# Kernel optimization log

Measured on AMD Instinct MI355X. Metric: run time of the kernel, lower is better.

## Reference

```python
import jax, jax.numpy as jnp
import numpy as np
from jax import lax

NAG = 3          # hardcoded in the torch module (query slices, catted_torches)
B = 4096         # batch_size per agent
H = 128          # hidden_dim
HEADS = 8
AD = H // HEADS  # attend_dim
STATE, ACT, SCAN = 48, 2, 256
OUTF, HID = 10, 256
NFEAT = 32 * (SCAN - 6)  # conv output features (two VALID convs: k5 then k3)
EPS = 1e-5

def leaky(x):
    return jnp.where(x >= 0, x, 0.01 * x)

def setup_inputs() -> dict:
    key = jax.random.key(0)
    ks = iter(jax.random.split(key, 40))
    def rn(shape, scale=0.05):
        return jax.random.normal(next(ks), shape, dtype=jnp.float32) * scale
    return {
        'obs':  jax.random.normal(next(ks), (NAG * B, STATE), jnp.float32),
        'acts': jax.random.normal(next(ks), (NAG * B, ACT), jnp.float32),
        'scan': jax.random.normal(next(ks), (NAG * B, SCAN), jnp.float32),
        'conv_w1': rn((32, 1, 5)),  'conv_b1': jnp.zeros((32,), jnp.float32),
        'conv_w2': rn((32, 32, 3)), 'conv_b2': jnp.zeros((32,), jnp.float32),
        'fc_w1': rn((256, NFEAT), 0.01), 'fc_b1': jnp.zeros((256,), jnp.float32),
        'fc_w2': rn((OUTF, 256)),        'fc_b2': jnp.zeros((OUTF,), jnp.float32),
        'enc_w': rn((H, STATE + ACT + OUTF)), 'enc_b': jnp.zeros((H,), jnp.float32),
        'Wk': rn((HEADS, AD, H)),
        'Wv': rn((HEADS, AD, H)), 'bv': jnp.zeros((HEADS, AD), jnp.float32),
        'Wq': rn((NAG, HEADS, AD, H)),
        'q1_w1': rn((HID, 2 * H)), 'q1_b1': jnp.zeros((HID,), jnp.float32),
        'q1_w2': rn((HID, HID)),   'q1_b2': jnp.zeros((HID,), jnp.float32),
        'q1_w3': rn((1, HID)),     'q1_b3': jnp.zeros((1,), jnp.float32),
        'q2_w1': rn((HID, 2 * H)), 'q2_b1': jnp.zeros((HID,), jnp.float32),
        'q2_w2': rn((HID, HID)),   'q2_b2': jnp.zeros((HID,), jnp.float32),
        'q2_w3': rn((1, HID)),     'q2_b3': jnp.zeros((1,), jnp.float32),
    }

def reference(obs, acts, scan, conv_w1, conv_b1, conv_w2, conv_b2,
              fc_w1, fc_b1, fc_w2, fc_b2, enc_w, enc_b, Wk, Wv, bv, Wq,
              q1_w1, q1_b1, q1_w2, q1_b2, q1_w3, q1_b3,
              q2_w1, q2_b1, q2_w2, q2_b2, q2_w3, q2_b3):
    dn = ('NCH', 'OIH', 'NCH')
    x = scan[:, None, :]                                            # [N,1,L]
    x = lax.conv_general_dilated(x, conv_w1, (1,), 'VALID', dimension_numbers=dn)
    x = jax.nn.relu(x + conv_b1[None, :, None])
    x = lax.conv_general_dilated(x, conv_w2, (1,), 'VALID', dimension_numbers=dn)
    x = jax.nn.relu(x + conv_b2[None, :, None])
    x = x.reshape(x.shape[0], -1)                                   # [N, NFEAT]
    x = jax.nn.relu(x @ fc_w1.T + fc_b1)
    feats = x @ fc_w2.T + fc_b2                                     # [N, OUTF]

    inps = jnp.concatenate([obs, acts, feats], axis=1)
    mu, var = inps.mean(0), inps.var(0)                             # BatchNorm1d (train, no affine)
    normed = (inps - mu) / jnp.sqrt(var + EPS)
    sa = leaky(normed @ enc_w.T + enc_b).reshape(NAG, B, H)         # [ag,B,H]

    keys = jnp.einsum('gbh,ndh->ngbd', sa, Wk)                      # [hd,ag,B,ad]
    vals = leaky(jnp.einsum('gbh,ndh->ngbd', sa, Wv) + bv[:, None, None, :])
    q = jnp.einsum('gbh,gndh->gnbd', sa, Wq)                        # [ag,hd,B,ad]

    logits = jnp.einsum('gnbd,nobd->gnbo', q, keys) / np.sqrt(AD)   # [ag,hd,B,ag]
    self_mask = jnp.eye(NAG, dtype=bool)[:, None, None, :]          # exclude own agent
    logits = jnp.where(self_mask, -jnp.inf, logits)
    w = jax.nn.softmax(logits, axis=-1)
    other = jnp.einsum('gnbo,nobd->gnbd', w, vals)                  # [ag,hd,B,ad]
    other = other.transpose(0, 2, 1, 3).reshape(NAG, B, H)          # heads concatenated

    emb = jnp.concatenate([sa, other], axis=2).reshape(NAG * B, 2 * H)

    def mlp(x, w1, b1, w2, b2, w3, b3):
        x = jax.nn.relu(x @ w1.T + b1)
        x = jax.nn.relu(x @ w2.T + b2)
        return x @ w3.T + b3

    q1 = mlp(emb, q1_w1, q1_b1, q1_w2, q1_b2, q1_w3, q1_b3)
    q2 = mlp(emb, q2_w1, q2_b1, q2_w2, q2_b2, q2_w3, q2_b3)
    return (q1, q2)
```

## Files before the change

kernel.cpp:

```cpp
#include <hip/hip_runtime.h>
#include <hip/hip_bf16.h>
#include <cstdint>
#include <cstddef>

typedef unsigned short u16;
typedef __attribute__((ext_vector_type(8))) __bf16 bf16x8;
typedef __attribute__((ext_vector_type(4))) float f32x4;

__device__ __forceinline__ u16 f2b(float f) {
  __hip_bfloat16 h = __float2bfloat16(f);
  return *reinterpret_cast<u16*>(&h);
}
__device__ __forceinline__ uint32_t pk2(float a, float b) {
  __hip_bfloat162 h = __float22bfloat162_rn(make_float2(a, b));
  return *reinterpret_cast<uint32_t*>(&h);
}
__device__ __forceinline__ float b2f(u16 u) {
  union { float f; uint32_t i; } x; x.i = ((uint32_t)u) << 16; return x.f;
}
__device__ __forceinline__ f32x4 mfma16(bf16x8 a, bf16x8 b, f32x4 c) {
  return __builtin_amdgcn_mfma_f32_16x16x32_bf16(a, b, c, 0, 0, 0);
}
__device__ __forceinline__ void async16(const void* g, void* l) {
  __builtin_amdgcn_global_load_lds((const __attribute__((address_space(1))) uint32_t*)g,
                                   (__attribute__((address_space(3))) uint32_t*)l, 16, 0, 0);
}

__global__ __launch_bounds__(256) void w1_perm(const float* __restrict__ w,
                                               u16* __restrict__ o) {
  __shared__ float L[8000];
  int j = blockIdx.x, tid = threadIdx.x;
  for (int i = tid; i < 8000; i += 256) L[i] = w[(size_t)j * 8000 + i];
  __syncthreads();
  for (int i = tid; i < 8000; i += 256) {
    int tt = i >> 5, cc = i & 31;
    int c2 = ((cc >> 2) & 1) * 16 + (cc >> 3) * 4 + (cc & 3);
    o[(size_t)j * 8000 + i] = f2b(L[c2 * 250 + tt]);
  }
}

struct CvtArgs {
  const float* src[15];
  void* dst[15];
  int cum[16];
  int kind[15];
};
__global__ __launch_bounds__(256) void f2b_multi(CvtArgs a, float* stats) {
  int i = blockIdx.x * 256 + threadIdx.x;
  if (blockIdx.x == 0 && threadIdx.x < 128) stats[threadIdx.x] = 0.f;
  int seg = 0;
  #pragma unroll
  for (int s = 1; s < 15; ++s) if (i >= a.cum[s]) seg = s;
  if (i < a.cum[15]) {
    int off = i - a.cum[seg];
    int kind = a.kind[seg];
    const float* src = a.src[seg];
    if (kind == 0) {
      ((u16*)a.dst[seg])[off] = f2b(src[off]);
    } else if (kind == 1) {
      int c2 = off / 96, rem = off - c2 * 96, kk = rem >> 5, c1 = rem & 31;
      ((u16*)a.dst[seg])[off] = f2b(src[(c2 * 32 + c1) * 3 + kk]);
    } else if (kind == 2) {
      int c1 = off >> 5, k = off & 31;
      ((u16*)a.dst[seg])[off] = f2b(k < 5 ? src[c1 * 5 + k] : 0.f);
    } else {
      ((float*)a.dst[seg])[off] = src[off];
    }
  }
}

__global__ __launch_bounds__(256) void conv_fused(
    const float* __restrict__ scan, const u16* __restrict__ w1g,
    const float* __restrict__ cb1, const u16* __restrict__ w2g,
    const float* __restrict__ cb2, u16* __restrict__ x) {
  __shared__ __align__(16) u16 A1[256 * 8];
  __shared__ __align__(16) u16 zbuf[4 * 8];
  __shared__ __align__(16) u16 h1T[258 * 40];
  int tid = threadIdx.x, lane = tid & 63, wv = tid >> 6;
  int l15 = lane & 15, quad = lane >> 4;
  const float* srow = scan + (size_t)blockIdx.x * 256;
  float sv[5];
  #pragma unroll
  for (int k = 0; k < 5; ++k) {
    int p = tid + k;
    sv[k] = (p < 256) ? srow[p] : 0.f;
  }
  union { bf16x8 v; uint32_t d[4]; } pk_;
  pk_.d[0] = pk2(sv[0], sv[1]);
  pk_.d[1] = pk2(sv[2], sv[3]);
  pk_.d[2] = pk2(sv[4], 0.f);
  pk_.d[3] = 0;
  *(bf16x8*)&A1[tid * 8] = pk_.v;
  if (lane < 8) zbuf[wv * 8 + lane] = 0;
  if (tid < 80) h1T[256 * 40 + tid] = 0;
  bf16x8 w1f[2];
  w1f[0] = *(const bf16x8*)&w1g[l15 * 32 + quad * 8];
  w1f[1] = *(const bf16x8*)&w1g[(16 + l15) * 32 + quad * 8];
  bf16x8 w2f[2][3];
  #pragma unroll
  for (int i = 0; i < 2; ++i)
    #pragma unroll
    for (int kk = 0; kk < 3; ++kk)
      w2f[i][kk] = *(const bf16x8*)&w2g[(i * 16 + l15) * 96 + kk * 32 + quad * 8];
  float cb1v[2][4], cb2v[2][4];
  #pragma unroll
  for (int i = 0; i < 2; ++i)
    #pragma unroll
    for (int r = 0; r < 4; ++r) {
      cb1v[i][r] = cb1[i * 16 + quad * 4 + r];
      cb2v[i][r] = cb2[i * 16 + quad * 4 + r];
    }
  asm volatile("s_waitcnt lgkmcnt(0)" ::: "memory");
  f32x4 zero = {0.f, 0.f, 0.f, 0.f};
  {
    f32x4 acc1[4][2];
    #pragma unroll
    for (int nt = 0; nt < 4; ++nt) { acc1[nt][0] = zero; acc1[nt][1] = zero; }
    #pragma unroll
    for (int nt = 0; nt < 4; ++nt) {
      int p = (wv * 4 + nt) * 16 + l15;
      const u16* bp = (quad == 0) ? &A1[p * 8] : &zbuf[wv * 8];
      bf16x8 bfr = *(const bf16x8*)bp;
      acc1[nt][0] = mfma16(w1f[0], bfr, acc1[nt][0]);
      acc1[nt][1] = mfma16(w1f[1], bfr, acc1[nt][1]);
    }
    #pragma unroll
    for (int nt = 0; nt < 4; ++nt) {
      int p = (wv * 4 + nt) * 16 + l15;
      #pragma unroll
      for (int mt = 0; mt < 2; ++mt) {
        float v0 = fmaxf(acc1[nt][mt][0] + cb1v[mt][0], 0.f);
        float v1 = fmaxf(acc1[nt][mt][1] + cb1v[mt][1], 0.f);
        float v2 = fmaxf(acc1[nt][mt][2] + cb1v[mt][2], 0.f);
        float v3 = fmaxf(acc1[nt][mt][3] + cb1v[mt][3], 0.f);
        uint2 u; u.x = pk2(v0, v1); u.y = pk2(v2, v3);
        *(uint2*)&h1T[p * 40 + mt * 16 + quad * 4] = u;
      }
    }
  }
  __syncthreads();
  f32x4 acc2[4][2];
  #pragma unroll
  for (int jj = 0; jj < 4; ++jj) { acc2[jj][0] = zero; acc2[jj][1] = zero; }
  #pragma unroll
  for (int kk = 0; kk < 3; ++kk) {
    #pragma unroll
    for (int jj = 0; jj < 4; ++jj) {
      int t = (wv * 4 + jj) * 16 + l15 + kk;
      bf16x8 h = *(const bf16x8*)&h1T[t * 40 + quad * 8];
      acc2[jj][0] = mfma16(w2f[0][kk], h, acc2[jj][0]);
      acc2[jj][1] = mfma16(w2f[1][kk], h, acc2[jj][1]);
    }
  }
  u16* xr = x + (size_t)blockIdx.x * 8000;
  #pragma unroll
  for (int jj = 0; jj < 4; ++jj) {
    int t = (wv * 4 + jj) * 16 + l15;
    if (t < 250) {
      union { bf16x8 v; uint32_t d[4]; } o_;
      #pragma unroll
      for (int i = 0; i < 2; ++i) {
        float v0 = fmaxf(acc2[jj][i][0] + cb2v[i][0], 0.f);
        float v1 = fmaxf(acc2[jj][i][1] + cb2v[i][1], 0.f);
        float v2 = fmaxf(acc2[jj][i][2] + cb2v[i][2], 0.f);
        float v3 = fmaxf(acc2[jj][i][3] + cb2v[i][3], 0.f);
        o_.d[i * 2]     = pk2(v0, v1);
        o_.d[i * 2 + 1] = pk2(v2, v3);
      }
      *(bf16x8*)&xr[t * 32 + quad * 8] = o_.v;
    }
  }
}

template <int MODE, int MROWS>
__global__ __launch_bounds__(256) void gemm_bt(
    const u16* __restrict__ A, int lda, const u16* __restrict__ W, int ldw,
    const float* __restrict__ bias, float* __restrict__ outF,
    u16* __restrict__ outB, int ldo, int nst, int a_sel, size_t out_zoff,
    const float* __restrict__ w3cat, float* __restrict__ pd) {
  constexpr int AI = (MROWS * 8) / 256;
  __shared__ __align__(16) u16 As[2][MROWS * 64];
  __shared__ __align__(16) u16 Bs[2][128 * 64];
  int tid = threadIdx.x;
  int m0 = blockIdx.y * MROWS;
  int sel = (MODE == 4) ? blockIdx.x : 0;
  int n0 = (MODE == 4) ? 0 : blockIdx.x * 128;
  if (MODE == 4) {
    size_t woff = (sel < 2) ? (size_t)sel * 128 : (size_t)(256 + (m0 >> 12) * 128);
    W += woff * 128;
    outB += (size_t)sel * 12288 * 128;
  }
  if (a_sel) A += (size_t)(blockIdx.x >> 1) * a_sel;
  int kbase = blockIdx.z * nst * 64;
  if (MODE == 0) outF += (size_t)blockIdx.z * out_zoff;
  const u16* Ap = A + (size_t)m0 * lda + kbase;
  const u16* Wp = W + (size_t)n0 * ldw + kbase;
  int lane = tid & 63, wv = tid >> 6;
  int l15 = lane & 15, quad = lane >> 4;
  int wm = (wv >> 1) * (MROWS / 2), wn = (wv & 1) * 64;
  constexpr int MI = MROWS / 32;
  f32x4 zero = {0.f, 0.f, 0.f, 0.f};
  f32x4 acc[MI][4];
  #pragma unroll
  for (int i = 0; i < MI; ++i)
    #pragma unroll
    for (int j = 0; j < 4; ++j) acc[i][j] = zero;

  int sraA[AI], sofA[AI], sdsA[AI];
  #pragma unroll
  for (int it = 0; it < AI; ++it) {
    int c = it * 256 + tid;
    int row = c >> 3, slot = c & 7;
    sraA[it] = row;
    sofA[it] = ((slot ^ (row & 7)) * 8);
    sdsA[it] = c * 8;
  }
  int sraW[4], sofW[4], sdsW[4];
  #pragma unroll
  for (int it = 0; it < 4; ++it) {
    int c = it * 256 + tid;
    int row = c >> 3, slot = c & 7;
    sraW[it] = row;
    sofW[it] = ((slot ^ (row & 7)) * 8);
    sdsW[it] = c * 8;
  }
  int rslot[2];
  rslot[0] = ((quad ^ (l15 & 7)) * 8);
  rslot[1] = (((4 + quad) ^ (l15 & 7)) * 8);

  #pragma unroll 1
  for (int st = 0; st < nst; ++st) {
    if (st == 0) {
      #pragma unroll
      for (int it = 0; it < AI; ++it)
        async16(Ap + (size_t)sraA[it] * lda + sofA[it], &As[0][sdsA[it]]);
      #pragma unroll
      for (int it = 0; it < 4; ++it)
        async16(Wp + (size_t)sraW[it] * ldw + sofW[it], &Bs[0][sdsW[it]]);
    }
    __syncthreads();
    if (st + 1 < nst) {
      const u16* An = Ap + (st + 1) * 64;
      const u16* Wn = Wp + (st + 1) * 64;
      u16* Ad = &As[(st + 1) & 1][0];
      u16* Bd = &Bs[(st + 1) & 1][0];
      #pragma unroll
      for (int it = 0; it < AI; ++it)
        async16(An + (size_t)sraA[it] * lda + sofA[it], Ad + sdsA[it]);
      #pragma unroll
      for (int it = 0; it < 4; ++it)
        async16(Wn + (size_t)sraW[it] * ldw + sofW[it], Bd + sdsW[it]);
    }
    const u16* Ab = &As[st & 1][0];
    const u16* Bb = &Bs[st & 1][0];
    #pragma unroll
    for (int s = 0; s < 2; ++s) {
      bf16x8 af[MI], bfr[4];
      #pragma unroll
      for (int i = 0; i < MI; ++i)
        af[i] = *(const bf16x8*)&Ab[(wm + i * 16 + l15) * 64 + rslot[s]];
      #pragma unroll
      for (int j = 0; j < 4; ++j)
        bfr[j] = *(const bf16x8*)&Bb[(wn + j * 16 + l15) * 64 + rslot[s]];
      #pragma unroll
      for (int i = 0; i < MI; ++i)
        #pragma unroll
        for (int j = 0; j < 4; ++j) acc[i][j] = mfma16(af[i], bfr[j], acc[i][j]);
    }
  }
  if (MODE == 5) {
    float w3v[4], bv4[4];
    #pragma unroll
    for (int j = 0; j < 4; ++j) {
      int n = n0 + wn + j * 16 + l15;
      w3v[j] = w3cat[n];
      bv4[j] = bias[n];
    }
    int sblk = (n0 >> 7) * 2 + (wv & 1);
    #pragma unroll
    for (int i = 0; i < MI; ++i) {
      int mb = m0 + wm + i * 16 + quad * 4;
      #pragma unroll
      for (int r = 0; r < 4; ++r) {
        float s = 0.f;
        #pragma unroll
        for (int j = 0; j < 4; ++j) {
          float v = fmaxf(acc[i][j][r] + bv4[j], 0.f);
          s += v * w3v[j];
        }
        s += __shfl_down(s, 8);
        s += __shfl_down(s, 4);
        s += __shfl_down(s, 2);
        s += __shfl_down(s, 1);
        if (l15 == 0) pd[(size_t)sblk * 12288 + mb + r] = s;
      }
    }
    return;
  }
  #pragma unroll
  for (int i = 0; i < MI; ++i) {
    int mb = m0 + wm + i * 16 + quad * 4;
    #pragma unroll
    for (int j = 0; j < 4; ++j) {
      int n = n0 + wn + j * 16 + l15;
      float bv_ = (MODE == 1 || MODE == 4) ? bias[n] : 0.f;
      #pragma unroll
      for (int r = 0; r < 4; ++r) {
        float v = acc[i][j][r];
        if (MODE == 0) {
          outF[(size_t)(mb + r) * ldo + n] = v;
        } else if (MODE == 1) {
          v = fmaxf(v + bv_, 0.f);
          outB[(size_t)(mb + r) * ldo + n] = f2b(v);
        } else {
          if (sel == 1) { v += bv_; v = v >= 0.f ? v : 0.01f * v; }
          outB[(size_t)(mb + r) * ldo + n] = f2b(v);
        }
      }
    }
  }
}

__global__ __launch_bounds__(256) void fc2_stats(
    const float* __restrict__ hparts, const float* __restrict__ b1,
    const float* __restrict__ w2, const float* __restrict__ b2,
    const float* __restrict__ obs, const float* __restrict__ acts,
    float* __restrict__ inps, float* __restrict__ stats) {
  __shared__ float hL[32 * 260];
  __shared__ float w2L[10 * 260];
  __shared__ float b1L[256];
  __shared__ float ipL[32 * 61];
  int tid = threadIdx.x, r0 = blockIdx.x * 32;
  b1L[tid] = b1[tid];
  for (int i = tid; i < 2560; i += 256) w2L[(i >> 8) * 260 + (i & 255)] = w2[i];
  for (int i = tid; i < 32 * 48; i += 256) {
    int r = i / 48, f = i - r * 48;
    ipL[r * 61 + f] = obs[(size_t)(r0 + r) * 48 + f];
  }
  if (tid < 64) {
    int r = tid >> 1, f = tid & 1;
    ipL[r * 61 + 48 + f] = acts[(size_t)(r0 + r) * 2 + f];
  }
  __syncthreads();
  const size_t HS = (size_t)12288 * 256;
  for (int i = tid; i < 32 * 256; i += 256) {
    int r = i >> 8, c = i & 255;
    size_t g = (size_t)(r0 + r) * 256 + c;
    float v = b1L[c] + hparts[g] + hparts[g + HS] + hparts[g + 2 * HS] +
              hparts[g + 3 * HS] + hparts[g + 4 * HS];
    hL[r * 260 + c] = fmaxf(v, 0.f);
  }
  __syncthreads();
  {
    int r = tid >> 3, ob = tid & 7;
    for (int o = ob; o < 10; o += 8) {
      float a = 0.f;
      #pragma unroll 8
      for (int c = 0; c < 256; ++c) a += hL[r * 260 + c] * w2L[o * 260 + c];
      ipL[r * 61 + 50 + o] = a + b2[o];
    }
  }
  __syncthreads();
  for (int i = tid; i < 32 * 60; i += 256) {
    int r = i / 60, f = i - r * 60;
    inps[(size_t)(r0 + r) * 64 + f] = ipL[r * 61 + f];
  }
  if (tid < 60) {
    float s = 0.f, s2 = 0.f;
    for (int r = 0; r < 32; ++r) {
      float v = ipL[r * 61 + tid];
      s += v; s2 += v * v;
    }
    atomicAdd(&stats[tid], s);
    atomicAdd(&stats[64 + tid], s2);
  }
}

__global__ __launch_bounds__(256) void enc_kernel(
    const float* __restrict__ inps, const float* __restrict__ stats,
    const float* __restrict__ enc_w, const float* __restrict__ enc_b,
    u16* __restrict__ sab) {
  __shared__ float ewL[128 * 61];
  __shared__ float nrm[32 * 61];
  __shared__ float ebL[128];
  __shared__ float muL[60], ivL[60];
  int tid = threadIdx.x, r0 = blockIdx.x * 32;
  if (tid < 128) ebL[tid] = enc_b[tid];
  if (tid < 60) {
    float s = stats[tid], s2 = stats[64 + tid];
    float mu = s * (1.f / 12288.f);
    float var = s2 * (1.f / 12288.f) - mu * mu;
    muL[tid] = mu;
    ivL[tid] = rsqrtf(var + 1e-5f);
  }
  for (int i = tid; i < 128 * 60; i += 256) {
    int h = i / 60, f = i - h * 60;
    ewL[h * 61 + f] = enc_w[i];
  }
  __syncthreads();
  for (int i = tid; i < 32 * 60; i += 256) {
    int r = i / 60, f = i - r * 60;
    nrm[r * 61 + f] = (inps[(size_t)(r0 + r) * 64 + f] - muL[f]) * ivL[f];
  }
  __syncthreads();
  for (int i = tid; i < 32 * 128; i += 256) {
    int r = i >> 7, h = i & 127;
    float a = ebL[h];
    #pragma unroll 4
    for (int f = 0; f < 60; ++f) a += nrm[r * 61 + f] * ewL[h * 61 + f];
    a = a >= 0.f ? a : 0.01f * a;
    sab[(size_t)(r0 + r) * 128 + h] = f2b(a);
  }
}

__global__ __launch_bounds__(128) void attn_combine(
    const u16* __restrict__ qb, const u16* __restrict__ keysb,
    const u16* __restrict__ valsb, const u16* __restrict__ sab,
    u16* __restrict__ emb) {
  __shared__ float qL[3][128], kL[3][128], vL[3][128];
  __shared__ float lg[3][8][3], wgt[3][8][3];
  int b = blockIdx.x, t = threadIdx.x;
  #pragma unroll
  for (int o = 0; o < 3; ++o) {
    size_t base = (size_t)(o * 4096 + b) * 128 + t;
    qL[o][t] = b2f(qb[base]);
    kL[o][t] = b2f(keysb[base]);
    vL[o][t] = b2f(valsb[base]);
  }
  __syncthreads();
  if (t < 72) {
    int g = t / 24, n = (t / 3) % 8, o = t % 3;
    float a = 0.f;
    #pragma unroll
    for (int d = 0; d < 16; ++d) a += qL[g][n * 16 + d] * kL[o][n * 16 + d];
    lg[g][n][o] = (o == g) ? -1e30f : a * 0.25f;
  }
  __syncthreads();
  if (t < 24) {
    int g = t / 8, n = t % 8;
    float m = fmaxf(fmaxf(lg[g][n][0], lg[g][n][1]), lg[g][n][2]);
    float e0 = expf(lg[g][n][0] - m), e1 = expf(lg[g][n][1] - m),
          e2 = expf(lg[g][n][2] - m);
    float inv = 1.f / (e0 + e1 + e2);
    wgt[g][n][0] = e0 * inv; wgt[g][n][1] = e1 * inv; wgt[g][n][2] = e2 * inv;
  }
  __syncthreads();
  int n = t >> 4, d = t & 15;
  #pragma unroll
  for (int g = 0; g < 3; ++g) {
    float o_ = wgt[g][n][0] * vL[0][n * 16 + d] +
               wgt[g][n][1] * vL[1][n * 16 + d] +
               wgt[g][n][2] * vL[2][n * 16 + d];
    size_t rbase = (size_t)(g * 4096 + b) * 256;
    emb[rbase + 128 + t] = f2b(o_);
    emb[rbase + t] = sab[(size_t)(g * 4096 + b) * 128 + t];
  }
}

__global__ __launch_bounds__(256) void final_sum(
    const float* __restrict__ pd, const float* __restrict__ b3a,
    const float* __restrict__ b3b, float* __restrict__ out) {
  int row = blockIdx.x * 256 + threadIdx.x;
  const size_t R = 12288;
  float s1 = pd[row] + pd[R + row] + pd[2 * R + row] + pd[3 * R + row];
  float s2 = pd[4 * R + row] + pd[5 * R + row] + pd[6 * R + row] + pd[7 * R + row];
  out[row] = s1 + b3a[0];
  out[R + row] = s2 + b3b[0];
}

extern "C" void kernel_launch(void* const* d_in, const int* in_sizes, int n_in,
                              void* d_out, int out_size, void* d_ws,
                              size_t ws_size, hipStream_t stream) {
  const float* obs  = (const float*)d_in[0];
  const float* acts = (const float*)d_in[1];
  const float* scan = (const float*)d_in[2];
  const float* cw1  = (const float*)d_in[3];
  const float* cb1  = (const float*)d_in[4];
  const float* cw2  = (const float*)d_in[5];
  const float* cb2  = (const float*)d_in[6];
  const float* fw1  = (const float*)d_in[7];
  const float* fb1  = (const float*)d_in[8];
  const float* fw2  = (const float*)d_in[9];
  const float* fb2  = (const float*)d_in[10];
  const float* encw = (const float*)d_in[11];
  const float* encb = (const float*)d_in[12];
  const float* Wk   = (const float*)d_in[13];
  const float* Wv   = (const float*)d_in[14];
  const float* bv   = (const float*)d_in[15];
  const float* Wq   = (const float*)d_in[16];
  const float* q1w1 = (const float*)d_in[17];
  const float* q1b1 = (const float*)d_in[18];
  const float* q1w2 = (const float*)d_in[19];
  const float* q1b2 = (const float*)d_in[20];
  const float* q1w3 = (const float*)d_in[21];
  const float* q1b3 = (const float*)d_in[22];
  const float* q2w1 = (const float*)d_in[23];
  const float* q2b1 = (const float*)d_in[24];
  const float* q2w2 = (const float*)d_in[25];
  const float* q2b2 = (const float*)d_in[26];
  const float* q2w3 = (const float*)d_in[27];
  const float* q2b3 = (const float*)d_in[28];
  float* out = (float*)d_out;
  char* ws = (char*)d_ws;
  if (ws_size < 264400000u) return;

  u16*   x     = (u16*)(ws + 0);
  u16*   w1b   = (u16*)(ws + 196608000);
  float* hpart = (float*)(ws + 200704000);
  float* stats = (float*)(ws + 263618560);
  u16*   wkvqb = (u16*)(ws + 263619584);
  u16*   m1ab  = (u16*)(ws + 263783424);
  u16*   m2ab  = (u16*)(ws + 264045568);
  u16*   w2g   = (u16*)(ws + 264307712);
  u16*   w1g   = (u16*)(ws + 264313856);
  float* bc1   = (float*)(ws + 264315904);
  float* bc2   = (float*)(ws + 264317952);
  float* w3cat = (float*)(ws + 264320000);
  float* inps  = (float*)(ws + 0);
  u16*   sab   = (u16*)(ws + 3145728);
  u16*   kvqb  = (u16*)(ws + 6291456);
  u16*   embb  = (u16*)(ws + 15728640);
  u16*   t1ab  = (u16*)(ws + 22020096);
  float* pd    = (float*)(ws + 34603008);
  u16*   keysb = kvqb;
  u16*   valsb = kvqb + (size_t)12288 * 128;
  u16*   qb    = kvqb + (size_t)2 * 12288 * 128;

  w1_perm<<<256, 256, 0, stream>>>(fw1, w1b);
  CvtArgs ca;
  const float* srcs[15] = {Wk, Wv, Wq, q1w1, q2w1, q1w2, q2w2, cw2, cw1,
                           q1b1, q2b1, q1b2, q2b2, q1w3, q2w3};
  void* dsts[15] = {wkvqb, wkvqb + 16384, wkvqb + 32768, m1ab, m1ab + 65536,
                    m2ab, m2ab + 65536, w2g, w1g, bc1, bc1 + 256, bc2,
                    bc2 + 256, w3cat, w3cat + 256};
  const int sz[15] = {16384, 16384, 49152, 65536, 65536, 65536, 65536,
                      3072, 1024, 256, 256, 256, 256, 256, 256};
  const int kinds[15] = {0, 0, 0, 0, 0, 0, 0, 1, 2, 3, 3, 3, 3, 3, 3};
  int cum = 0;
  ca.cum[0] = 0;
  for (int i = 0; i < 15; ++i) {
    ca.src[i] = srcs[i]; ca.dst[i] = dsts[i]; ca.kind[i] = kinds[i];
    cum += sz[i]; ca.cum[i + 1] = cum;
  }
  f2b_multi<<<(cum + 255) / 256, 256, 0, stream>>>(ca, stats);

  conv_fused<<<12288, 256, 0, stream>>>(scan, w1g, cb1, w2g, cb2, x);
  gemm_bt<0, 128><<<dim3(2, 96, 5), 256, 0, stream>>>(
      x, 8000, w1b, 8000, nullptr, hpart, nullptr, 256, 25, 0,
      (size_t)12288 * 256, nullptr, nullptr);
  fc2_stats<<<384, 256, 0, stream>>>(hpart, fb1, fw2, fb2, obs, acts, inps, stats);
  enc_kernel<<<384, 256, 0, stream>>>(inps, stats, encw, encb, sab);
  gemm_bt<4, 64><<<dim3(3, 192, 1), 256, 0, stream>>>(
      sab, 128, wkvqb, 128, bv, nullptr, kvqb, 128, 2, 0, 0, nullptr, nullptr);
  attn_combine<<<4096, 128, 0, stream>>>(qb, keysb, valsb, sab, embb);
  gemm_bt<1, 64><<<dim3(4, 192, 1), 256, 0, stream>>>(
      embb, 256, m1ab, 256, bc1, nullptr, t1ab, 512, 4, 0, 0, nullptr, nullptr);
  gemm_bt<5, 64><<<dim3(4, 192, 1), 256, 0, stream>>>(
      t1ab, 512, m2ab, 256, bc2, nullptr, nullptr, 0, 4, 256, 0, w3cat, pd);
  final_sum<<<48, 256, 0, stream>>>(pd, q1b3, q2b3, out);
}
```

Measured before the change: 364.7 us.

## Fuse conv layers into FC1 GEMM, computing conv activations on the fly

Replaces the separate conv kernel, which wrote a large bf16 activation tensor to global memory, and the following split-K FC1 GEMM with one fused kernel. Each block computes conv1 and conv2 for its 64 rows on the fly with a rolling 4-column buffer in LDS, stages the result in shared memory, and multiplies it against the FC1 weights read directly from global memory. This removes the roughly 200MB intermediate write and read. In exchange, the conv work is recomputed for each of the two N-blocks, the weight loads are not staged through LDS or double-buffered, and there are two barriers per k-step.

Measured after the change: 460.4 us. 26.2% more time.

```diff
diff --git a/kernel.cpp b/kernel.cpp
--- a/kernel.cpp
+++ b/kernel.cpp
@@ -69,30 +69,18 @@
   }
 }
 
-__global__ __launch_bounds__(256) void conv_fused(
+__global__ __launch_bounds__(256) void convfc1(
     const float* __restrict__ scan, const u16* __restrict__ w1g,
     const float* __restrict__ cb1, const u16* __restrict__ w2g,
-    const float* __restrict__ cb2, u16* __restrict__ x) {
-  __shared__ __align__(16) u16 A1[256 * 8];
-  __shared__ __align__(16) u16 zbuf[4 * 8];
-  __shared__ __align__(16) u16 h1T[258 * 40];
+    const float* __restrict__ cb2, const u16* __restrict__ w1b,
+    float* __restrict__ hpart) {
+  __shared__ __align__(16) u16 h1w[4][4 * 16 * 40];
+  __shared__ __align__(16) u16 Xs[64 * 72];
   int tid = threadIdx.x, lane = tid & 63, wv = tid >> 6;
   int l15 = lane & 15, quad = lane >> 4;
-  const float* srow = scan + (size_t)blockIdx.x * 256;
-  float sv[5];
-  #pragma unroll
-  for (int k = 0; k < 5; ++k) {
-    int p = tid + k;
-    sv[k] = (p < 256) ? srow[p] : 0.f;
-  }
-  union { bf16x8 v; uint32_t d[4]; } pk_;
-  pk_.d[0] = pk2(sv[0], sv[1]);
-  pk_.d[1] = pk2(sv[2], sv[3]);
-  pk_.d[2] = pk2(sv[4], 0.f);
-  pk_.d[3] = 0;
-  *(bf16x8*)&A1[tid * 8] = pk_.v;
-  if (lane < 8) zbuf[wv * 8 + lane] = 0;
-  if (tid < 80) h1T[256 * 40 + tid] = 0;
+  int m0 = blockIdx.y * 64, n0 = blockIdx.x * 128, z = blockIdx.z;
+  int t0 = z * 50;
+  f32x4 zero = {0.f, 0.f, 0.f, 0.f};
   bf16x8 w1f[2];
   w1f[0] = *(const bf16x8*)&w1g[l15 * 32 + quad * 8];
   w1f[1] = *(const bf16x8*)&w1g[(16 + l15) * 32 + quad * 8];
@@ -110,64 +98,116 @@
       cb1v[i][r] = cb1[i * 16 + quad * 4 + r];
       cb2v[i][r] = cb2[i * 16 + quad * 4 + r];
     }
-  asm volatile("s_waitcnt lgkmcnt(0)" ::: "memory");
-  f32x4 zero = {0.f, 0.f, 0.f, 0.f};
-  {
-    f32x4 acc1[4][2];
-    #pragma unroll
-    for (int nt = 0; nt < 4; ++nt) { acc1[nt][0] = zero; acc1[nt][1] = zero; }
-    #pragma unroll
-    for (int nt = 0; nt < 4; ++nt) {
-      int p = (wv * 4 + nt) * 16 + l15;
-      const u16* bp = (quad == 0) ? &A1[p * 8] : &zbuf[wv * 8];
-      bf16x8 bfr = *(const bf16x8*)bp;
-      acc1[nt][0] = mfma16(w1f[0], bfr, acc1[nt][0]);
-      acc1[nt][1] = mfma16(w1f[1], bfr, acc1[nt][1]);
-    }
-    #pragma unroll
-    for (int nt = 0; nt < 4; ++nt) {
-      int p = (wv * 4 + nt) * 16 + l15;
-      #pragma unroll
-      for (int mt = 0; mt < 2; ++mt) {
-        float v0 = fmaxf(acc1[nt][mt][0] + cb1v[mt][0], 0.f);
-        float v1 = fmaxf(acc1[nt][mt][1] + cb1v[mt][1], 0.f);
-        float v2 = fmaxf(acc1[nt][mt][2] + cb1v[mt][2], 0.f);
-        float v3 = fmaxf(acc1[nt][mt][3] + cb1v[mt][3], 0.f);
-        uint2 u; u.x = pk2(v0, v1); u.y = pk2(v2, v3);
-        *(uint2*)&h1T[p * 40 + mt * 16 + quad * 4] = u;
+  const float* srow = scan + (size_t)(m0 + wv * 16 + l15) * 256;
+  float sreg[5];
+  if (quad == 0) {
+    #pragma unroll
+    for (int k = 0; k < 5; ++k) sreg[k] = srow[t0 + k];
+  }
+  u16* myh1 = &h1w[wv][0];
+  int h1wo = l15 * 40 + quad * 4;
+  int h1ro = l15 * 40 + quad * 8;
+
+  auto conv1_col = [&](int p) {
+    union { bf16x8 v; uint32_t d[4]; } u;
+    uint32_t d0 = pk2(sreg[0], sreg[1]);
+    uint32_t d1 = pk2(sreg[2], sreg[3]);
+    uint32_t d2 = pk2(sreg[4], 0.f);
+    u.d[0] = (quad == 0) ? d0 : 0u;
+    u.d[1] = (quad == 0) ? d1 : 0u;
+    u.d[2] = (quad == 0) ? d2 : 0u;
+    u.d[3] = 0u;
+    f32x4 a0 = mfma16(w1f[0], u.v, zero);
+    f32x4 a1 = mfma16(w1f[1], u.v, zero);
+    int sb = (p & 3) * 640;
+    #pragma unroll
+    for (int mt = 0; mt < 2; ++mt) {
+      f32x4 a = mt ? a1 : a0;
+      float v0 = fmaxf(a[0] + cb1v[mt][0], 0.f);
+      float v1 = fmaxf(a[1] + cb1v[mt][1], 0.f);
+      float v2 = fmaxf(a[2] + cb1v[mt][2], 0.f);
+      float v3 = fmaxf(a[3] + cb1v[mt][3], 0.f);
+      uint2 w; w.x = pk2(v0, v1); w.y = pk2(v2, v3);
+      *(uint2*)&myh1[sb + h1wo + mt * 16] = w;
+    }
+    if (quad == 0) {
+      sreg[0] = sreg[1]; sreg[1] = sreg[2]; sreg[2] = sreg[3]; sreg[3] = sreg[4];
+      int nx = p + 5;
+      sreg[4] = srow[nx < 256 ? nx : 255];
+    }
+  };
+  conv1_col(t0);
+  conv1_col(t0 + 1);
+
+  int wm = (wv >> 1) * 32, wn = (wv & 1) * 64;
+  f32x4 acc[2][4];
+  #pragma unroll
+  for (int i = 0; i < 2; ++i)
+    #pragma unroll
+    for (int j = 0; j < 4; ++j) acc[i][j] = zero;
+  int xw = (wv * 16 + l15) * 72 + quad * 8;
+  const u16* Wb = w1b + (size_t)z * 1600 + quad * 8;
+
+  #pragma unroll 1
+  for (int st = 0; st < 25; ++st) {
+    int t = t0 + st * 2;
+    conv1_col(t + 2);
+    conv1_col(t + 3);
+    bf16x8 xo[2];
+    #pragma unroll
+    for (int s = 0; s < 2; ++s) {
+      f32x4 c0 = zero, c1 = zero;
+      #pragma unroll
+      for (int kk = 0; kk < 3; ++kk) {
+        bf16x8 h = *(const bf16x8*)&myh1[((t + s + kk) & 3) * 640 + h1ro];
+        c0 = mfma16(w2f[0][kk], h, c0);
+        c1 = mfma16(w2f[1][kk], h, c1);
       }
-    }
-  }
-  __syncthreads();
-  f32x4 acc2[4][2];
-  #pragma unroll
-  for (int jj = 0; jj < 4; ++jj) { acc2[jj][0] = zero; acc2[jj][1] = zero; }
-  #pragma unroll
-  for (int kk = 0; kk < 3; ++kk) {
-    #pragma unroll
-    for (int jj = 0; jj < 4; ++jj) {
-      int t = (wv * 4 + jj) * 16 + l15 + kk;
-      bf16x8 h = *(const bf16x8*)&h1T[t * 40 + quad * 8];
-      acc2[jj][0] = mfma16(w2f[0][kk], h, acc2[jj][0]);
-      acc2[jj][1] = mfma16(w2f[1][kk], h, acc2[jj][1]);
-    }
-  }
-  u16* xr = x + (size_t)blockIdx.x * 8000;
-  #pragma unroll
-  for (int jj = 0; jj < 4; ++jj) {
-    int t = (wv * 4 + jj) * 16 + l15;
-    if (t < 250) {
       union { bf16x8 v; uint32_t d[4]; } o_;
-      #pragma unroll
-      for (int i = 0; i < 2; ++i) {
-        float v0 = fmaxf(acc2[jj][i][0] + cb2v[i][0], 0.f);
-        float v1 = fmaxf(acc2[jj][i][1] + cb2v[i][1], 0.f);
-        float v2 = fmaxf(acc2[jj][i][2] + cb2v[i][2], 0.f);
-        float v3 = fmaxf(acc2[jj][i][3] + cb2v[i][3], 0.f);
-        o_.d[i * 2]     = pk2(v0, v1);
-        o_.d[i * 2 + 1] = pk2(v2, v3);
+      {
+        float v0 = fmaxf(c0[0] + cb2v[0][0], 0.f);
+        float v1 = fmaxf(c0[1] + cb2v[0][1], 0.f);
+        float v2 = fmaxf(c0[2] + cb2v[0][2], 0.f);
+        float v3 = fmaxf(c0[3] + cb2v[0][3], 0.f);
+        o_.d[0] = pk2(v0, v1); o_.d[1] = pk2(v2, v3);
+        float w0 = fmaxf(c1[0] + cb2v[1][0], 0.f);
+        float w1 = fmaxf(c1[1] + cb2v[1][1], 0.f);
+        float w2 = fmaxf(c1[2] + cb2v[1][2], 0.f);
+        float w3 = fmaxf(c1[3] + cb2v[1][3], 0.f);
+        o_.d[2] = pk2(w0, w1); o_.d[3] = pk2(w2, w3);
       }
-      *(bf16x8*)&xr[t * 32 + quad * 8] = o_.v;
+      xo[s] = o_.v;
+    }
+    __syncthreads();
+    *(bf16x8*)&Xs[xw] = xo[0];
+    *(bf16x8*)&Xs[xw + 32] = xo[1];
+    __syncthreads();
+    #pragma unroll
+    for (int s = 0; s < 2; ++s) {
+      int kc = (st * 2 + s) * 32;
+      bf16x8 af[2], bfr[4];
+      #pragma unroll
+      for (int i = 0; i < 2; ++i)
+        af[i] = *(const bf16x8*)&Xs[(wm + i * 16 + l15) * 72 + s * 32 + quad * 8];
+      #pragma unroll
+      for (int j = 0; j < 4; ++j)
+        bfr[j] = *(const bf16x8*)(Wb + (size_t)(n0 + wn + j * 16 + l15) * 8000 + kc);
+      #pragma unroll
+      for (int i = 0; i < 2; ++i)
+        #pragma unroll
+        for (int j = 0; j < 4; ++j) acc[i][j] = mfma16(af[i], bfr[j], acc[i][j]);
+    }
+  }
+  hpart += (size_t)z * 12288 * 256;
+  #pragma unroll
+  for (int i = 0; i < 2; ++i) {
+    int mb = m0 + wm + i * 16 + quad * 4;
+    #pragma unroll
+    for (int j = 0; j < 4; ++j) {
+      int n = n0 + wn + j * 16 + l15;
+      #pragma unroll
+      for (int r = 0; r < 4; ++r)
+        hpart[(size_t)(mb + r) * 256 + n] = acc[i][j][r];
     }
   }
 }
@@ -504,7 +544,6 @@
   char* ws = (char*)d_ws;
   if (ws_size < 264400000u) return;
 
-  u16*   x     = (u16*)(ws + 0);
   u16*   w1b   = (u16*)(ws + 196608000);
   float* hpart = (float*)(ws + 200704000);
   float* stats = (float*)(ws + 263618560);
@@ -544,10 +583,8 @@
   }
   f2b_multi<<<(cum + 255) / 256, 256, 0, stream>>>(ca, stats);
 
-  conv_fused<<<12288, 256, 0, stream>>>(scan, w1g, cb1, w2g, cb2, x);
-  gemm_bt<0, 128><<<dim3(2, 96, 5), 256, 0, stream>>>(
-      x, 8000, w1b, 8000, nullptr, hpart, nullptr, 256, 25, 0,
-      (size_t)12288 * 256, nullptr, nullptr);
+  convfc1<<<dim3(2, 192, 5), 256, 0, stream>>>(scan, w1g, cb1, w2g, cb2, w1b,
+                                               hpart);
   fc2_stats<<<384, 256, 0, stream>>>(hpart, fb1, fw2, fb2, obs, acts, inps, stats);
   enc_kernel<<<384, 256, 0, stream>>>(inps, stats, encw, encb, sab);
   gemm_bt<4, 64><<<dim3(3, 192, 1), 256, 0, stream>>>(
```
